# Performance work log

Hardware: AMD Instinct MI355X
Metric: run time of the kernel (lower is better)

Reference implementation:

```python
import jax, jax.numpy as jnp
import numpy as np

MIN_SCALE = 0.05
MAX_SCALE = 0.2
EPS = 0.001
RATE = 4
SUBSAMPLE = 3


def box_filter(x, k):
    # matches torch: pad (1+p) before / p after on H and W, double cumsum + subtract
    if k % 2 == 0:
        k = k + 1
    p = k // 2
    xp = jnp.pad(x, ((0, 0), (0, 0), (1 + p, p), (1 + p, p)))
    c = jnp.cumsum(xp, axis=2)
    y = c[:, :, k:, :] - c[:, :, :-k, :]
    c2 = jnp.cumsum(y, axis=3)
    return c2[:, :, :, k:] - c2[:, :, :, :-k]


def _resize(x, h, w):
    # torch F.interpolate(mode='bilinear', align_corners=False) == jax bilinear, no antialias
    n, c = x.shape[0], x.shape[1]
    return jax.image.resize(x, (n, c, h, w), method='bilinear', antialias=False)


def rf_norm(x):
    N, C, H, W = x.shape
    scale = MAX_SCALE
    it = 1
    while True:  # loop bounds depend only on static config -> Python loop is jit-safe
        win = int(max(H, W) * scale)
        if win < 3 and it == 1:
            mean = x.mean(axis=(1, 2, 3), keepdims=True)
            std = x.std(axis=(1, 2, 3), ddof=1, keepdims=True) + EPS
            x = x / std - mean / std
        else:
            if SUBSAMPLE > 1 and min(H, W) > SUBSAMPLE * 10 and win > SUBSAMPLE * 5:
                xs = _resize(x, H // SUBSAMPLE, W // SUBSAMPLE)
                win = win // SUBSAMPLE
            else:
                xs = x
            h, w = xs.shape[2], xs.shape[3]
            ones = jnp.ones((1, 1, h, w), x.dtype)
            M = box_filter(ones, win)
            x_mean = box_filter(xs, win).mean(axis=1, keepdims=True) / M
            x2_mean = box_filter(xs ** 2, win).mean(axis=1, keepdims=True) / M
            var = jnp.clip(x2_mean - x_mean ** 2, 0.0) + EPS
            std = jnp.sqrt(var)
            a = 1.0 / std
            b = -x_mean / std
            mean_a = box_filter(a, win) / M
            mean_b = box_filter(b, win) / M
            if SUBSAMPLE > 1:
                mean_a = _resize(mean_a, H, W)
                mean_b = _resize(mean_b, H, W)
            x = mean_a * x + mean_b
        it += 1
        scale /= RATE  # coarse_to_fine=True
        if scale < MIN_SCALE:
            break
    return x


def setup_inputs() -> dict:
    key = jax.random.key(0)
    x = jax.random.normal(key, (16, 3, 768, 768), dtype=jnp.float32)
    return {"x": x}


def reference(x):
    return rf_norm(x)
```

## Files before the change

### kernel.cpp

```cpp
#include <hip/hip_runtime.h>


#define N_B 16
#define CCH 3
#define HF 768
#define HL 256
#define SLICE (HL * HL)
#define TOT_L (N_B * SLICE)
#define EPSV 1e-3f

__device__ __forceinline__ int cnt(int i, int P) {
  int hi = i + P; if (hi > HL - 1) hi = HL - 1;
  int lo = i - P; if (lo < 0) lo = 0;
  return hi - lo + 1;
}

template <int P, int G>
__device__ __forceinline__ void hbox2g(float a, float b, int g, int j,
    float (*s0)[HL], float (*s1)[HL], float (*wtA)[4], float (*wtB)[4],
    float& ra, float& rb) {
  int lane = j & 63, w = j >> 6;
  __syncthreads();
#pragma unroll
  for (int d = 1; d < 64; d <<= 1) {
    float ta = __shfl_up(a, (unsigned)d);
    float tb = __shfl_up(b, (unsigned)d);
    if (lane >= d) { a += ta; b += tb; }
  }
  if (lane == 63) { wtA[g][w] = a; wtB[g][w] = b; }
  __syncthreads();
  float offa = 0.f, offb = 0.f;
  for (int ww = 0; ww < w; ++ww) { offa += wtA[g][ww]; offb += wtB[g][ww]; }
  s0[g][j] = a + offa;
  s1[g][j] = b + offb;
  __syncthreads();
  int hi = j + P; if (hi > HL - 1) hi = HL - 1;
  int lo = j - P - 1;
  ra = s0[g][hi]; rb = s1[g][hi];
  if (lo >= 0) { ra -= s0[g][lo]; rb -= s1[g][lo]; }
}

__device__ __forceinline__ void xpose_write4(float ra, float rb, int g, int j,
    int tid, float (*s0)[HL], float (*s1)[HL],
    float* __restrict__ d0, float* __restrict__ d1, size_t nb, int col0) {
  __syncthreads();
  s0[g][j] = ra; s1[g][j] = rb;
  __syncthreads();
  if (tid < HL) {
    float4 va, vb;
    va.x = s0[0][tid]; va.y = s0[1][tid]; va.z = s0[2][tid]; va.w = s0[3][tid];
    vb.x = s1[0][tid]; vb.y = s1[1][tid]; vb.z = s1[2][tid]; vb.w = s1[3][tid];
    *(float4*)(d0 + nb + (size_t)tid * HL + col0) = va;
    *(float4*)(d1 + nb + (size_t)tid * HL + col0) = vb;
  }
}

__global__ __launch_bounds__(1024) void k1(const float* __restrict__ x,
    float* __restrict__ u, float* __restrict__ v,
    float* __restrict__ S0, float* __restrict__ S1) {
  __shared__ float stage[4][HF];
  __shared__ float s0[4][HL], s1[4][HL];
  __shared__ float wtA[4][4], wtB[4][4];
  int b = blockIdx.x;
  int n = b >> 6;
  int ib = (b & 63) << 2;
  int tid = threadIdx.x;
  int g = tid >> 8, j = tid & 255;
  int srow = tid / 192, scol = (tid % 192) * 4;
  float ua = 0.f, va = 0.f;
  const size_t imgbase = (size_t)n * CCH * HF * HF;
  for (int c = 0; c < CCH; ++c) {
    __syncthreads();
    if (tid < 768) {
      const float* src = x + imgbase + (size_t)c * HF * HF
                       + (size_t)(3 * (ib + srow) + 1) * HF + scol;
      *(float4*)&stage[srow][scol] = *(const float4*)src;
    }
    __syncthreads();
    float val = stage[g][3 * j + 1];
    ua += val;
    va += val * val;
  }
  float uu = ua * (1.f / 3.f), vv = va * (1.f / 3.f);
  size_t nb = (size_t)n * SLICE;
  size_t base = nb + (size_t)(ib + g) * HL;
  u[base + j] = uu;
  v[base + j] = vv;
  float ra, rb;
  hbox2g<25, 4>(uu, vv, g, j, s0, s1, wtA, wtB, ra, rb);
  xpose_write4(ra, rb, g, j, tid, s0, s1, S0, S1, nb, ib);
}

__global__ __launch_bounds__(1024) void k2(const float* __restrict__ S0,
    const float* __restrict__ S1, float* __restrict__ P0,
    float* __restrict__ P1) {
  __shared__ float s0[4][HL], s1[4][HL];
  __shared__ float wtA[4][4], wtB[4][4];
  int n = blockIdx.x >> 6, strip = blockIdx.x & 63;
  int tid = threadIdx.x, g = tid >> 8, j = tid & 255;
  int c = strip * 4 + g;
  size_t nb = (size_t)n * SLICE;
  float sa = S0[nb + (size_t)c * HL + j];
  float sb = S1[nb + (size_t)c * HL + j];
  float bu, bv;
  hbox2g<25, 4>(sa, sb, g, j, s0, s1, wtA, wtB, bu, bv);
  float invM = 1.f / ((float)cnt(j, 25) * (float)cnt(c, 25));
  float xm = bu * invM, x2m = bv * invM;
  float var = x2m - xm * xm; if (var < 0.f) var = 0.f;
  float inv = 1.f / sqrtf(var + EPSV);
  float av = inv, bv2 = -xm * inv;
  float ra, rb;
  hbox2g<25, 4>(av, bv2, g, j, s0, s1, wtA, wtB, ra, rb);
  xpose_write4(ra, rb, g, j, tid, s0, s1, P0, P1, nb, strip * 4);
}

__global__ __launch_bounds__(1024) void k3(const float* __restrict__ P0,
    const float* __restrict__ P1, const float* __restrict__ u,
    const float* __restrict__ v, float* __restrict__ A1,
    float* __restrict__ B1, float* __restrict__ Q0, float* __restrict__ Q1) {
  __shared__ float s0[4][HL], s1[4][HL];
  __shared__ float wtA[4][4], wtB[4][4];
  int n = blockIdx.x >> 6, strip = blockIdx.x & 63;
  int tid = threadIdx.x, g = tid >> 8, j = tid & 255;
  int i = strip * 4 + g;
  size_t nb = (size_t)n * SLICE;
  size_t idx = nb + (size_t)i * HL + j;
  float pa = P0[idx], pb = P1[idx];
  float ba, bb;
  hbox2g<25, 4>(pa, pb, g, j, s0, s1, wtA, wtB, ba, bb);
  float invM = 1.f / ((float)cnt(i, 25) * (float)cnt(j, 25));
  float Av = ba * invM, Bv = bb * invM;
  A1[idx] = Av;
  B1[idx] = Bv;
  float un = u[idx], vn = v[idx];
  float u2 = Av * un + Bv;
  float v2 = Av * Av * vn + 2.f * Av * Bv * un + Bv * Bv;
  float ra, rb;
  hbox2g<6, 4>(u2, v2, g, j, s0, s1, wtA, wtB, ra, rb);
  xpose_write4(ra, rb, g, j, tid, s0, s1, Q0, Q1, nb, strip * 4);
}

__global__ __launch_bounds__(1024) void k4(const float* __restrict__ Q0,
    const float* __restrict__ Q1, float* __restrict__ R0,
    float* __restrict__ R1) {
  __shared__ float s0[4][HL], s1[4][HL];
  __shared__ float wtA[4][4], wtB[4][4];
  int n = blockIdx.x >> 6, strip = blockIdx.x & 63;
  int tid = threadIdx.x, g = tid >> 8, j = tid & 255;
  int c = strip * 4 + g;
  size_t nb = (size_t)n * SLICE;
  float qa = Q0[nb + (size_t)c * HL + j];
  float qb = Q1[nb + (size_t)c * HL + j];
  float bu, bv;
  hbox2g<6, 4>(qa, qb, g, j, s0, s1, wtA, wtB, bu, bv);
  float invM = 1.f / ((float)cnt(j, 6) * (float)cnt(c, 6));
  float xm = bu * invM, x2m = bv * invM;
  float var = x2m - xm * xm; if (var < 0.f) var = 0.f;
  float inv = 1.f / sqrtf(var + EPSV);
  float av = inv, bv2 = -xm * inv;
  float ra, rb;
  hbox2g<6, 4>(av, bv2, g, j, s0, s1, wtA, wtB, ra, rb);
  xpose_write4(ra, rb, g, j, tid, s0, s1, R0, R1, nb, strip * 4);
}

__device__ __forceinline__ void upw(int q, int& i0, int& i1, float& w1) {
  int d = q / 3;
  int r = q - 3 * d;
  if (r == 1) { i0 = d; i1 = d; w1 = 0.f; }
  else if (r == 2) { i0 = d; i1 = d + 1; if (i1 > HL - 1) i1 = HL - 1; w1 = 1.f / 3.f; }
  else { i1 = d; i0 = d - 1; if (i0 < 0) i0 = 0; w1 = 2.f / 3.f; }
}

__global__ __launch_bounds__(256) void k_final(
    const float* __restrict__ x, const float* __restrict__ A1m,
    const float* __restrict__ B1m, const float* __restrict__ R0,
    const float* __restrict__ R1, float* __restrict__ out) {
  __shared__ float ry[4][HL];
  __shared__ float s0[1][HL], s1[1][HL];
  __shared__ float wtA[1][4], wtB[1][4];
  int nb_ = blockIdx.x;
  int y = nb_ % HF;
  int n = nb_ / HF;
  int t = threadIdx.x;
  int iy0, iy1;
  float wy1;
  upw(y, iy0, iy1, wy1);
  float wy0 = 1.f - wy1;
  size_t mb = (size_t)n * SLICE;
  ry[0][t] = wy0 * A1m[mb + (size_t)iy0 * HL + t] + wy1 * A1m[mb + (size_t)iy1 * HL + t];
  ry[1][t] = wy0 * B1m[mb + (size_t)iy0 * HL + t] + wy1 * B1m[mb + (size_t)iy1 * HL + t];
  float cj6 = (float)cnt(t, 6);
  float ra, rb;
  hbox2g<6, 1>(R0[mb + (size_t)iy0 * HL + t], R1[mb + (size_t)iy0 * HL + t],
               0, t, s0, s1, wtA, wtB, ra, rb);
  float inv0 = 1.f / ((float)cnt(iy0, 6) * cj6);
  float A20 = ra * inv0, B20 = rb * inv0;
  hbox2g<6, 1>(R0[mb + (size_t)iy1 * HL + t], R1[mb + (size_t)iy1 * HL + t],
               0, t, s0, s1, wtA, wtB, ra, rb);
  float inv1 = 1.f / ((float)cnt(iy1, 6) * cj6);
  ry[2][t] = wy0 * A20 + wy1 * (ra * inv1);
  ry[3][t] = wy0 * B20 + wy1 * (rb * inv1);
  __syncthreads();
  if (t < 192) {
    float A1c[4], B1c[4], A2c[4], B2c[4];
#pragma unroll
    for (int e = 0; e < 4; ++e) {
      int q = 4 * t + e;
      int ix0, ix1;
      float wx1;
      upw(q, ix0, ix1, wx1);
      float wx0 = 1.f - wx1;
      A1c[e] = wx0 * ry[0][ix0] + wx1 * ry[0][ix1];
      B1c[e] = wx0 * ry[1][ix0] + wx1 * ry[1][ix1];
      A2c[e] = wx0 * ry[2][ix0] + wx1 * ry[2][ix1];
      B2c[e] = wx0 * ry[3][ix0] + wx1 * ry[3][ix1];
    }
    size_t rowbase = ((size_t)(n * CCH) * HF + y) * HF + 4 * t;
#pragma unroll
    for (int c = 0; c < CCH; ++c) {
      const float4 xin = *(const float4*)(x + rowbase + (size_t)c * HF * HF);
      float4 o;
      o.x = A2c[0] * (A1c[0] * xin.x + B1c[0]) + B2c[0];
      o.y = A2c[1] * (A1c[1] * xin.y + B1c[1]) + B2c[1];
      o.z = A2c[2] * (A1c[2] * xin.z + B1c[2]) + B2c[2];
      o.w = A2c[3] * (A1c[3] * xin.w + B1c[3]) + B2c[3];
      *(float4*)(out + rowbase + (size_t)c * HF * HF) = o;
    }
  }
}

extern "C" void kernel_launch(void* const* d_in, const int* in_sizes, int n_in,
                              void* d_out, int out_size, void* d_ws, size_t ws_size,
                              hipStream_t stream) {
  const float* x = (const float*)d_in[0];
  float* out = (float*)d_out;
  const size_t S = (size_t)TOT_L;
  float* wsf = (float*)d_ws;
  float *u, *v, *S0, *S1, *P0, *P1, *A1, *B1, *R0, *R1, *Q0, *Q1;
  if (ws_size >= 10 * S * sizeof(float)) {
    u = wsf;      v = u + S;   S0 = v + S;   S1 = S0 + S;  P0 = S1 + S;
    P1 = P0 + S;  A1 = P1 + S; B1 = A1 + S;  R0 = B1 + S;  R1 = R0 + S;
  } else {
    A1 = wsf; B1 = A1 + S; R0 = B1 + S; R1 = R0 + S;
    u = out; v = u + S; S0 = v + S; S1 = S0 + S; P0 = S1 + S; P1 = P0 + S;
  }
  Q0 = S0; Q1 = S1;

  k1<<<N_B * 64, 1024, 0, stream>>>(x, u, v, S0, S1);
  k2<<<N_B * 64, 1024, 0, stream>>>(S0, S1, P0, P1);
  k3<<<N_B * 64, 1024, 0, stream>>>(P0, P1, u, v, A1, B1, Q0, Q1);
  k4<<<N_B * 64, 1024, 0, stream>>>(Q0, Q1, R0, R1);
  k_final<<<N_B * HF, 256, 0, stream>>>(x, A1, B1, R0, R1, out);
}
```

Measured before the change: 105.1 us.

## Interleave paired intermediate planes as float2 and fuse box subtract into transposed store

Stores each pair of intermediate planes (u/v, S0/S1, P, A1/B1, R) as interleaved float2 arrays instead of two separate float planes. Each thread's paired loads and stores become a single 8-byte access. The scan now keeps prefix sums in shared memory, and the box-window subtraction is done inside the transposed store. This removes one extra shared-memory write and barrier round per stage. The trade-offs are 8-byte strided shared-memory accesses, which can raise bank conflicts, and more indexing work in the store threads.

```diff
diff --git a/kernel.cpp b/kernel.cpp
--- a/kernel.cpp
+++ b/kernel.cpp
@@ -15,10 +15,8 @@
   return hi - lo + 1;
 }
 
-template <int P, int G>
-__device__ __forceinline__ void hbox2g(float a, float b, int g, int j,
-    float (*s0)[HL], float (*s1)[HL], float (*wtA)[4], float (*wtB)[4],
-    float& ra, float& rb) {
+__device__ __forceinline__ void scan2g(float a, float b, int g, int j,
+    float2 (*s)[HL], float2 (*wt)[4]) {
   int lane = j & 63, w = j >> 6;
   __syncthreads();
 #pragma unroll
@@ -27,40 +25,42 @@
     float tb = __shfl_up(b, (unsigned)d);
     if (lane >= d) { a += ta; b += tb; }
   }
-  if (lane == 63) { wtA[g][w] = a; wtB[g][w] = b; }
+  if (lane == 63) wt[g][w] = make_float2(a, b);
   __syncthreads();
   float offa = 0.f, offb = 0.f;
-  for (int ww = 0; ww < w; ++ww) { offa += wtA[g][ww]; offb += wtB[g][ww]; }
-  s0[g][j] = a + offa;
-  s1[g][j] = b + offb;
-  __syncthreads();
+  for (int ww = 0; ww < w; ++ww) { float2 t = wt[g][ww]; offa += t.x; offb += t.y; }
+  s[g][j] = make_float2(a + offa, b + offb);
+  __syncthreads();
+}
+
+template <int P>
+__device__ __forceinline__ float2 boxr(const float2 (*s)[HL], int g, int j) {
   int hi = j + P; if (hi > HL - 1) hi = HL - 1;
   int lo = j - P - 1;
-  ra = s0[g][hi]; rb = s1[g][hi];
-  if (lo >= 0) { ra -= s0[g][lo]; rb -= s1[g][lo]; }
-}
-
-__device__ __forceinline__ void xpose_write4(float ra, float rb, int g, int j,
-    int tid, float (*s0)[HL], float (*s1)[HL],
-    float* __restrict__ d0, float* __restrict__ d1, size_t nb, int col0) {
-  __syncthreads();
-  s0[g][j] = ra; s1[g][j] = rb;
-  __syncthreads();
+  float2 r = s[g][hi];
+  if (lo >= 0) { float2 l = s[g][lo]; r.x -= l.x; r.y -= l.y; }
+  return r;
+}
+
+template <int P>
+__device__ __forceinline__ void xpose_store(const float2 (*s)[HL], int tid,
+    float2* __restrict__ dst, size_t nb, int col0) {
   if (tid < HL) {
-    float4 va, vb;
-    va.x = s0[0][tid]; va.y = s0[1][tid]; va.z = s0[2][tid]; va.w = s0[3][tid];
-    vb.x = s1[0][tid]; vb.y = s1[1][tid]; vb.z = s1[2][tid]; vb.w = s1[3][tid];
-    *(float4*)(d0 + nb + (size_t)tid * HL + col0) = va;
-    *(float4*)(d1 + nb + (size_t)tid * HL + col0) = vb;
+    float2 r0 = boxr<P>(s, 0, tid);
+    float2 r1 = boxr<P>(s, 1, tid);
+    float2 r2 = boxr<P>(s, 2, tid);
+    float2 r3 = boxr<P>(s, 3, tid);
+    float4* d = (float4*)(dst + nb + (size_t)tid * HL + col0);
+    d[0] = make_float4(r0.x, r0.y, r1.x, r1.y);
+    d[1] = make_float4(r2.x, r2.y, r3.x, r3.y);
   }
 }
 
 __global__ __launch_bounds__(1024) void k1(const float* __restrict__ x,
-    float* __restrict__ u, float* __restrict__ v,
-    float* __restrict__ S0, float* __restrict__ S1) {
+    float2* __restrict__ UV, float2* __restrict__ Spk) {
   __shared__ float stage[4][HF];
-  __shared__ float s0[4][HL], s1[4][HL];
-  __shared__ float wtA[4][4], wtB[4][4];
+  __shared__ float2 s[4][HL];
+  __shared__ float2 wt[4][4];
   int b = blockIdx.x;
   int n = b >> 6;
   int ib = (b & 63) << 2;
@@ -83,84 +83,70 @@
   }
   float uu = ua * (1.f / 3.f), vv = va * (1.f / 3.f);
   size_t nb = (size_t)n * SLICE;
-  size_t base = nb + (size_t)(ib + g) * HL;
-  u[base + j] = uu;
-  v[base + j] = vv;
-  float ra, rb;
-  hbox2g<25, 4>(uu, vv, g, j, s0, s1, wtA, wtB, ra, rb);
-  xpose_write4(ra, rb, g, j, tid, s0, s1, S0, S1, nb, ib);
-}
-
-__global__ __launch_bounds__(1024) void k2(const float* __restrict__ S0,
-    const float* __restrict__ S1, float* __restrict__ P0,
-    float* __restrict__ P1) {
-  __shared__ float s0[4][HL], s1[4][HL];
-  __shared__ float wtA[4][4], wtB[4][4];
+  UV[nb + (size_t)(ib + g) * HL + j] = make_float2(uu, vv);
+  scan2g(uu, vv, g, j, s, wt);
+  xpose_store<25>(s, tid, Spk, nb, ib);
+}
+
+__global__ __launch_bounds__(1024) void k2(const float2* __restrict__ Spk,
+    float2* __restrict__ Ppk) {
+  __shared__ float2 s[4][HL];
+  __shared__ float2 wt[4][4];
   int n = blockIdx.x >> 6, strip = blockIdx.x & 63;
   int tid = threadIdx.x, g = tid >> 8, j = tid & 255;
   int c = strip * 4 + g;
   size_t nb = (size_t)n * SLICE;
-  float sa = S0[nb + (size_t)c * HL + j];
-  float sb = S1[nb + (size_t)c * HL + j];
-  float bu, bv;
-  hbox2g<25, 4>(sa, sb, g, j, s0, s1, wtA, wtB, bu, bv);
+  float2 sv = Spk[nb + (size_t)c * HL + j];
+  scan2g(sv.x, sv.y, g, j, s, wt);
+  float2 bu = boxr<25>(s, g, j);
   float invM = 1.f / ((float)cnt(j, 25) * (float)cnt(c, 25));
-  float xm = bu * invM, x2m = bv * invM;
+  float xm = bu.x * invM, x2m = bu.y * invM;
   float var = x2m - xm * xm; if (var < 0.f) var = 0.f;
   float inv = 1.f / sqrtf(var + EPSV);
-  float av = inv, bv2 = -xm * inv;
-  float ra, rb;
-  hbox2g<25, 4>(av, bv2, g, j, s0, s1, wtA, wtB, ra, rb);
-  xpose_write4(ra, rb, g, j, tid, s0, s1, P0, P1, nb, strip * 4);
-}
-
-__global__ __launch_bounds__(1024) void k3(const float* __restrict__ P0,
-    const float* __restrict__ P1, const float* __restrict__ u,
-    const float* __restrict__ v, float* __restrict__ A1,
-    float* __restrict__ B1, float* __restrict__ Q0, float* __restrict__ Q1) {
-  __shared__ float s0[4][HL], s1[4][HL];
-  __shared__ float wtA[4][4], wtB[4][4];
+  scan2g(inv, -xm * inv, g, j, s, wt);
+  xpose_store<25>(s, tid, Ppk, nb, strip * 4);
+}
+
+__global__ __launch_bounds__(1024) void k3(const float2* __restrict__ Ppk,
+    const float2* __restrict__ UV, float2* __restrict__ AB1,
+    float2* __restrict__ Qpk) {
+  __shared__ float2 s[4][HL];
+  __shared__ float2 wt[4][4];
   int n = blockIdx.x >> 6, strip = blockIdx.x & 63;
   int tid = threadIdx.x, g = tid >> 8, j = tid & 255;
   int i = strip * 4 + g;
   size_t nb = (size_t)n * SLICE;
   size_t idx = nb + (size_t)i * HL + j;
-  float pa = P0[idx], pb = P1[idx];
-  float ba, bb;
-  hbox2g<25, 4>(pa, pb, g, j, s0, s1, wtA, wtB, ba, bb);
+  float2 pv = Ppk[idx];
+  scan2g(pv.x, pv.y, g, j, s, wt);
+  float2 bb = boxr<25>(s, g, j);
   float invM = 1.f / ((float)cnt(i, 25) * (float)cnt(j, 25));
-  float Av = ba * invM, Bv = bb * invM;
-  A1[idx] = Av;
-  B1[idx] = Bv;
-  float un = u[idx], vn = v[idx];
-  float u2 = Av * un + Bv;
-  float v2 = Av * Av * vn + 2.f * Av * Bv * un + Bv * Bv;
-  float ra, rb;
-  hbox2g<6, 4>(u2, v2, g, j, s0, s1, wtA, wtB, ra, rb);
-  xpose_write4(ra, rb, g, j, tid, s0, s1, Q0, Q1, nb, strip * 4);
-}
-
-__global__ __launch_bounds__(1024) void k4(const float* __restrict__ Q0,
-    const float* __restrict__ Q1, float* __restrict__ R0,
-    float* __restrict__ R1) {
-  __shared__ float s0[4][HL], s1[4][HL];
-  __shared__ float wtA[4][4], wtB[4][4];
+  float Av = bb.x * invM, Bv = bb.y * invM;
+  AB1[idx] = make_float2(Av, Bv);
+  float2 uv = UV[idx];
+  float u2 = Av * uv.x + Bv;
+  float v2 = Av * Av * uv.y + 2.f * Av * Bv * uv.x + Bv * Bv;
+  scan2g(u2, v2, g, j, s, wt);
+  xpose_store<6>(s, tid, Qpk, nb, strip * 4);
+}
+
+__global__ __launch_bounds__(1024) void k4(const float2* __restrict__ Qpk,
+    float2* __restrict__ Rpk) {
+  __shared__ float2 s[4][HL];
+  __shared__ float2 wt[4][4];
   int n = blockIdx.x >> 6, strip = blockIdx.x & 63;
   int tid = threadIdx.x, g = tid >> 8, j = tid & 255;
   int c = strip * 4 + g;
   size_t nb = (size_t)n * SLICE;
-  float qa = Q0[nb + (size_t)c * HL + j];
-  float qb = Q1[nb + (size_t)c * HL + j];
-  float bu, bv;
-  hbox2g<6, 4>(qa, qb, g, j, s0, s1, wtA, wtB, bu, bv);
+  float2 qv = Qpk[nb + (size_t)c * HL + j];
+  scan2g(qv.x, qv.y, g, j, s, wt);
+  float2 bu = boxr<6>(s, g, j);
   float invM = 1.f / ((float)cnt(j, 6) * (float)cnt(c, 6));
-  float xm = bu * invM, x2m = bv * invM;
+  float xm = bu.x * invM, x2m = bu.y * invM;
   float var = x2m - xm * xm; if (var < 0.f) var = 0.f;
   float inv = 1.f / sqrtf(var + EPSV);
-  float av = inv, bv2 = -xm * inv;
-  float ra, rb;
-  hbox2g<6, 4>(av, bv2, g, j, s0, s1, wtA, wtB, ra, rb);
-  xpose_write4(ra, rb, g, j, tid, s0, s1, R0, R1, nb, strip * 4);
+  scan2g(inv, -xm * inv, g, j, s, wt);
+  xpose_store<6>(s, tid, Rpk, nb, strip * 4);
 }
 
 __device__ __forceinline__ void upw(int q, int& i0, int& i1, float& w1) {
@@ -172,12 +158,11 @@
 }
 
 __global__ __launch_bounds__(256) void k_final(
-    const float* __restrict__ x, const float* __restrict__ A1m,
-    const float* __restrict__ B1m, const float* __restrict__ R0,
-    const float* __restrict__ R1, float* __restrict__ out) {
-  __shared__ float ry[4][HL];
-  __shared__ float s0[1][HL], s1[1][HL];
-  __shared__ float wtA[1][4], wtB[1][4];
+    const float* __restrict__ x, const float2* __restrict__ AB1,
+    const float2* __restrict__ Rpk, float* __restrict__ out) {
+  __shared__ float2 ry01[HL], ry23[HL];
+  __shared__ float2 s[1][HL];
+  __shared__ float2 wt[1][4];
   int nb_ = blockIdx.x;
   int y = nb_ % HF;
   int n = nb_ / HF;
@@ -187,19 +172,21 @@
   upw(y, iy0, iy1, wy1);
   float wy0 = 1.f - wy1;
   size_t mb = (size_t)n * SLICE;
-  ry[0][t] = wy0 * A1m[mb + (size_t)iy0 * HL + t] + wy1 * A1m[mb + (size_t)iy1 * HL + t];
-  ry[1][t] = wy0 * B1m[mb + (size_t)iy0 * HL + t] + wy1 * B1m[mb + (size_t)iy1 * HL + t];
+  float2 a0 = AB1[mb + (size_t)iy0 * HL + t];
+  float2 a1 = AB1[mb + (size_t)iy1 * HL + t];
+  ry01[t] = make_float2(wy0 * a0.x + wy1 * a1.x, wy0 * a0.y + wy1 * a1.y);
   float cj6 = (float)cnt(t, 6);
-  float ra, rb;
-  hbox2g<6, 1>(R0[mb + (size_t)iy0 * HL + t], R1[mb + (size_t)iy0 * HL + t],
-               0, t, s0, s1, wtA, wtB, ra, rb);
+  float2 r0v = Rpk[mb + (size_t)iy0 * HL + t];
+  scan2g(r0v.x, r0v.y, 0, t, s, wt);
+  float2 b0 = boxr<6>(s, 0, t);
   float inv0 = 1.f / ((float)cnt(iy0, 6) * cj6);
-  float A20 = ra * inv0, B20 = rb * inv0;
-  hbox2g<6, 1>(R0[mb + (size_t)iy1 * HL + t], R1[mb + (size_t)iy1 * HL + t],
-               0, t, s0, s1, wtA, wtB, ra, rb);
+  float A20 = b0.x * inv0, B20 = b0.y * inv0;
+  float2 r1v = Rpk[mb + (size_t)iy1 * HL + t];
+  scan2g(r1v.x, r1v.y, 0, t, s, wt);
+  float2 b1 = boxr<6>(s, 0, t);
   float inv1 = 1.f / ((float)cnt(iy1, 6) * cj6);
-  ry[2][t] = wy0 * A20 + wy1 * (ra * inv1);
-  ry[3][t] = wy0 * B20 + wy1 * (rb * inv1);
+  ry23[t] = make_float2(wy0 * A20 + wy1 * b1.x * inv1,
+                        wy0 * B20 + wy1 * b1.y * inv1);
   __syncthreads();
   if (t < 192) {
     float A1c[4], B1c[4], A2c[4], B2c[4];
@@ -210,10 +197,12 @@
       float wx1;
       upw(q, ix0, ix1, wx1);
       float wx0 = 1.f - wx1;
-      A1c[e] = wx0 * ry[0][ix0] + wx1 * ry[0][ix1];
-      B1c[e] = wx0 * ry[1][ix0] + wx1 * ry[1][ix1];
-      A2c[e] = wx0 * ry[2][ix0] + wx1 * ry[2][ix1];
-      B2c[e] = wx0 * ry[3][ix0] + wx1 * ry[3][ix1];
+      float2 m0 = ry01[ix0], m1 = ry01[ix1];
+      float2 m2 = ry23[ix0], m3 = ry23[ix1];
+      A1c[e] = wx0 * m0.x + wx1 * m1.x;
+      B1c[e] = wx0 * m0.y + wx1 * m1.y;
+      A2c[e] = wx0 * m2.x + wx1 * m3.x;
+      B2c[e] = wx0 * m2.y + wx1 * m3.y;
     }
     size_t rowbase = ((size_t)(n * CCH) * HF + y) * HF + 4 * t;
 #pragma unroll
@@ -235,20 +224,19 @@
   const float* x = (const float*)d_in[0];
   float* out = (float*)d_out;
   const size_t S = (size_t)TOT_L;
-  float* wsf = (float*)d_ws;
-  float *u, *v, *S0, *S1, *P0, *P1, *A1, *B1, *R0, *R1, *Q0, *Q1;
+  float2 *UV, *Spk, *Ppk, *AB1, *Rpk, *Qpk;
   if (ws_size >= 10 * S * sizeof(float)) {
-    u = wsf;      v = u + S;   S0 = v + S;   S1 = S0 + S;  P0 = S1 + S;
-    P1 = P0 + S;  A1 = P1 + S; B1 = A1 + S;  R0 = B1 + S;  R1 = R0 + S;
+    float2* w = (float2*)d_ws;
+    UV = w; Spk = UV + S; Ppk = Spk + S; AB1 = Ppk + S; Rpk = AB1 + S;
   } else {
-    A1 = wsf; B1 = A1 + S; R0 = B1 + S; R1 = R0 + S;
-    u = out; v = u + S; S0 = v + S; S1 = S0 + S; P0 = S1 + S; P1 = P0 + S;
-  }
-  Q0 = S0; Q1 = S1;
-
-  k1<<<N_B * 64, 1024, 0, stream>>>(x, u, v, S0, S1);
-  k2<<<N_B * 64, 1024, 0, stream>>>(S0, S1, P0, P1);
-  k3<<<N_B * 64, 1024, 0, stream>>>(P0, P1, u, v, A1, B1, Q0, Q1);
-  k4<<<N_B * 64, 1024, 0, stream>>>(Q0, Q1, R0, R1);
-  k_final<<<N_B * HF, 256, 0, stream>>>(x, A1, B1, R0, R1, out);
-}
+    AB1 = (float2*)d_ws; Rpk = AB1 + S;
+    UV = (float2*)out; Spk = UV + S; Ppk = Spk + S;
+  }
+  Qpk = Spk;
+
+  k1<<<N_B * 64, 1024, 0, stream>>>(x, UV, Spk);
+  k2<<<N_B * 64, 1024, 0, stream>>>(Spk, Ppk);
+  k3<<<N_B * 64, 1024, 0, stream>>>(Ppk, UV, AB1, Qpk);
+  k4<<<N_B * 64, 1024, 0, stream>>>(Qpk, Rpk);
+  k_final<<<N_B * HF, 256, 0, stream>>>(x, AB1, Rpk, out);
+}
```

Result: faster. 99.11 us (-5.7%).
